# Kernel optimization log

Hardware: AMD Instinct MI355X
Metric: run time of the kernel (lower is better)

Reference implementation:

```python
import jax, jax.numpy as jnp
import numpy as np


def setup_inputs() -> dict:
    key = jax.random.key(0)
    k1, k2, k3, k4 = jax.random.split(key, 4)
    B, C_in, E = 8, 32, 100000
    C_out, K = 64, 5
    x = jax.random.normal(k1, (B, C_in, E, 1), dtype=jnp.float32)
    gemm_edges = jax.random.randint(k2, (B, E, 4), 0, E, dtype=jnp.int32)
    fan_in = C_in * K
    weight = jax.random.normal(k3, (C_out, C_in, 1, K), dtype=jnp.float32) / np.sqrt(fan_in)
    bias = jax.random.normal(k4, (C_out,), dtype=jnp.float32) * 0.01
    return {"x": x, "gemm_edges": gemm_edges, "weight": weight, "bias": bias}


def reference(x, gemm_edges, weight, bias):
    # x: (B, C, E, 1) edge features; gemm_edges: (B, E, 4) ring-neighbor indices
    xs = x[..., 0]                                   # (B, C, E)
    B, C, E = xs.shape
    # prepend self index -> (B, E, 5); +1 shifts into padded table (slot 0 = zero pad)
    idx_self = jnp.broadcast_to(jnp.arange(E, dtype=gemm_edges.dtype)[None, :, None], (B, E, 1))
    Gi = jnp.concatenate([idx_self, gemm_edges], axis=2) + 1  # (B, E, 5)
    xp = jnp.pad(xs, ((0, 0), (0, 0), (1, 0)))       # (B, C, E+1) with zero column at index 0
    # per-batch gather: f[b, c, e, k] = xp[b, c, Gi[b, e, k]]
    f = jnp.take_along_axis(xp, Gi.reshape(B, 1, E * 5), axis=2).reshape(B, C, E, 5)
    f0, f1, f2, f3, f4 = (f[..., i] for i in range(5))
    # symmetric functions for neighbor-order invariance
    G = jnp.stack([f0, f1 + f3, f2 + f4, jnp.abs(f1 - f3), jnp.abs(f2 - f4)], axis=3)  # (B, C, E, 5)
    # Conv2d kernel (1, 5) == contraction over (C, k), output (B, C_out, E, 1)
    out = jnp.einsum('bcek,ock->boe', G, weight[:, :, 0, :]) + bias[None, :, None]
    return out[..., None]
```

## Files before the change

### kernel.cpp

```cpp
#include <hip/hip_runtime.h>
#include <stdint.h>

#define E_TOTAL 100000
#define B_TOTAL 8
#define CIN 32
#define COUT 64
#define TILES 1563

typedef short bf16x8 __attribute__((ext_vector_type(8)));
typedef float f32x4  __attribute__((ext_vector_type(4)));
typedef int   i32x4  __attribute__((ext_vector_type(4)));
typedef unsigned u32x4 __attribute__((ext_vector_type(4)));

union U16x8 { u32x4 u; bf16x8 s; };

__device__ inline float blo(unsigned u) { return __uint_as_float(u << 16); }
__device__ inline float bhi(unsigned u) { return __uint_as_float(u & 0xffff0000u); }
__device__ inline unsigned bpack(float lo, float hi) {
    return (__float_as_uint(lo) >> 16) | (__float_as_uint(hi) & 0xffff0000u);
}
__device__ inline unsigned badd(unsigned a, unsigned b) {
    return bpack(blo(a) + blo(b), bhi(a) + bhi(b));
}
__device__ inline unsigned babsdiff(unsigned a, unsigned b) {
    return bpack(fabsf(blo(a) - blo(b)), fabsf(bhi(a) - bhi(b)));
}
__device__ inline u32x4 vadd4(u32x4 a, u32x4 b) {
    u32x4 r;
#pragma unroll
    for (int i = 0; i < 4; i++) r[i] = badd(a[i], b[i]);
    return r;
}
__device__ inline u32x4 vabsdiff4(u32x4 a, u32x4 b) {
    u32x4 r;
#pragma unroll
    for (int i = 0; i < 4; i++) r[i] = babsdiff(a[i], b[i]);
    return r;
}
__device__ inline unsigned rne16(float f) {
    unsigned b = __float_as_uint(f);
    b += 0x7fffu + ((b >> 16) & 1u);
    return b >> 16;
}

__global__ __launch_bounds__(256) void prep_transpose(
    const float* __restrict__ x, unsigned* __restrict__ xt,
    const float* __restrict__ w, unsigned short* __restrict__ wb) {
    const int tid = threadIdx.x;
    if (blockIdx.x >= TILES * 8) {
        for (int idx = tid; idx < 4 * 5 * 64 * 8; idx += 256) {
            int j = idx & 7;
            int lane = (idx >> 3) & 63;
            int tg = idx >> 9;
            int g = tg % 5;
            int t = tg / 5;
            int n = lane & 15, qq = lane >> 4;
            int o = n + 16 * t;
            int c = qq * 8 + j;
            wb[idx] = (unsigned short)rne16(w[(o * CIN + c) * 5 + g]);
        }
        return;
    }
    __shared__ float tbuf[CIN][65];
    const int b = blockIdx.x & 7;
    const int e0 = (blockIdx.x >> 3) * 64;
    const int el = tid & 63;
    const int cw = tid >> 6;
#pragma unroll
    for (int i = 0; i < 8; i++) {
        int c = cw * 8 + i;
        int e = e0 + el;
        float v = (e < E_TOTAL)
            ? __builtin_nontemporal_load(x + ((size_t)b * CIN + c) * E_TOTAL + e)
            : 0.f;
        tbuf[c][el] = v;
    }
    __syncthreads();
    const int c2 = tid & 15;
#pragma unroll
    for (int i = 0; i < 4; i++) {
        int el2 = (tid >> 4) * 4 + i;
        int e = e0 + el2;
        if (e < E_TOTAL) {
            unsigned lo = rne16(tbuf[c2 * 2][el2]);
            unsigned hi = rne16(tbuf[c2 * 2 + 1][el2]);
            xt[((size_t)b * E_TOTAL + e) * 16 + c2] = lo | (hi << 16);
        }
    }
}

__global__ __launch_bounds__(256) void meshconv_main(
    const unsigned short* __restrict__ xt,
    const int* __restrict__ ge,
    const u32x4* __restrict__ wb,
    const float* __restrict__ bias,
    float* __restrict__ out) {
    __shared__ u32x4 wlds[1280];
    const int tid = threadIdx.x;
    const int lane = tid & 63;
    const int wv = tid >> 6;
    const int b = blockIdx.x & 7;
    const int tile = blockIdx.x >> 3;
    const int e0 = tile * 64 + wv * 16;
    const int n = lane & 15;
    const int q = lane >> 4;
    const bool active = (e0 < E_TOTAL);
    const int em = active ? (e0 + n) : 0;

    i32x4 nid = __builtin_nontemporal_load(
        (const i32x4*)(ge + ((size_t)b * E_TOTAL + em) * 4));
    const unsigned short* xb = xt + (size_t)b * E_TOTAL * CIN;
    const int co = q * 8;
    u32x4 a0 = *(const u32x4*)(xb + (size_t)em * CIN + co);

#pragma unroll
    for (int k = 0; k < 5; k++) wlds[tid + k * 256] = wb[tid + k * 256];
    __syncthreads();

    u32x4 a1 = *(const u32x4*)(xb + (size_t)nid[0] * CIN + co);
    u32x4 a2 = *(const u32x4*)(xb + (size_t)nid[1] * CIN + co);
    u32x4 a3 = *(const u32x4*)(xb + (size_t)nid[2] * CIN + co);
    u32x4 a4 = *(const u32x4*)(xb + (size_t)nid[3] * CIN + co);

    u32x4 A[5];
    A[0] = a0;
    A[1] = vadd4(a1, a3);
    A[2] = vadd4(a2, a4);
    A[3] = vabsdiff4(a1, a3);
    A[4] = vabsdiff4(a2, a4);

    f32x4 acc[4];
#pragma unroll
    for (int t = 0; t < 4; t++)
#pragma unroll
        for (int r = 0; r < 4; r++) acc[t][r] = 0.f;

#pragma unroll
    for (int g = 0; g < 5; g++) {
        U16x8 av; av.u = A[g];
#pragma unroll
        for (int t = 0; t < 4; t++) {
            U16x8 bv; bv.u = wlds[(t * 5 + g) * 64 + lane];
            acc[t] = __builtin_amdgcn_mfma_f32_16x16x32_bf16(av.s, bv.s, acc[t], 0, 0, 0);
        }
    }

    if (active) {
#pragma unroll
        for (int t = 0; t < 4; t++) {
            const int o = n + 16 * t;
            f32x4 r = acc[t] + bias[o];
            __builtin_nontemporal_store(
                r, (f32x4*)(out + ((size_t)b * COUT + o) * E_TOTAL + e0 + q * 4));
        }
    }
}

__global__ __launch_bounds__(256) void meshconv_fallback(
    const float* __restrict__ x, const int* __restrict__ ge,
    const float* __restrict__ w, const float* __restrict__ bias,
    float* __restrict__ out) {
    __shared__ float f[5][32];
    __shared__ float G[5][32];
    __shared__ int idxs[4];
    const int e = blockIdx.x, b = blockIdx.y;
    const int tid = threadIdx.x;
    if (tid < 4) idxs[tid] = ge[((size_t)b * E_TOTAL + e) * 4 + tid];
    __syncthreads();
    if (tid < 160) {
        int k = tid >> 5, c = tid & 31;
        int src = (k == 0) ? e : idxs[k - 1];
        f[k][c] = x[((size_t)b * CIN + c) * E_TOTAL + src];
    }
    __syncthreads();
    if (tid < 32) {
        int c = tid;
        G[0][c] = f[0][c];
        G[1][c] = f[1][c] + f[3][c];
        G[2][c] = f[2][c] + f[4][c];
        G[3][c] = fabsf(f[1][c] - f[3][c]);
        G[4][c] = fabsf(f[2][c] - f[4][c]);
    }
    __syncthreads();
    if (tid < COUT) {
        float acc = bias[tid];
        for (int c = 0; c < CIN; c++)
#pragma unroll
            for (int g = 0; g < 5; g++)
                acc += G[g][c] * w[(tid * CIN + c) * 5 + g];
        out[((size_t)b * COUT + tid) * E_TOTAL + e] = acc;
    }
}

extern "C" void kernel_launch(void* const* d_in, const int* in_sizes, int n_in,
                              void* d_out, int out_size, void* d_ws, size_t ws_size,
                              hipStream_t stream) {
    const float* x = (const float*)d_in[0];
    const int* ge = (const int*)d_in[1];
    const float* w = (const float*)d_in[2];
    const float* bias = (const float*)d_in[3];
    float* out = (float*)d_out;

    const size_t xt_bytes = (size_t)B_TOTAL * E_TOTAL * CIN * 2;
    const size_t need = 65536 + xt_bytes;
    if (ws_size < need) {
        dim3 grid(E_TOTAL, B_TOTAL);
        meshconv_fallback<<<grid, 256, 0, stream>>>(x, ge, w, bias, out);
        return;
    }
    unsigned short* wb = (unsigned short*)d_ws;
    unsigned short* xt = (unsigned short*)((char*)d_ws + 65536);

    prep_transpose<<<TILES * 8 + 1, 256, 0, stream>>>(x, (unsigned*)xt, w, wb);
    meshconv_main<<<TILES * 8, 256, 0, stream>>>(xt, ge, (const u32x4*)wb, bias, out);
}
```

Before: 393.2 us.

## Make meshconv main kernel persistent with software-prefetched index and self loads

Replaces the one-tile-per-block launch with a persistent grid of 256 blocks per batch that loops over 128-edge units. Each wave now handles two 16-edge groups per iteration and prefetches the next unit's neighbor indices and self features while gathering the current ones. The weight LDS fill is paid once per block instead of once per tile. The cost is a much smaller grid and more live registers, which may reduce latency hiding for the random gathers.

```diff
diff --git a/kernel.cpp b/kernel.cpp
--- a/kernel.cpp
+++ b/kernel.cpp
@@ -6,6 +6,8 @@
 #define CIN 32
 #define COUT 64
 #define TILES 1563
+#define NUNITS 782
+#define NBLK 256
 
 typedef short bf16x8 __attribute__((ext_vector_type(8)));
 typedef float f32x4  __attribute__((ext_vector_type(4)));
@@ -54,8 +56,8 @@
             int tg = idx >> 9;
             int g = tg % 5;
             int t = tg / 5;
-            int n = lane & 15, qq = lane >> 4;
-            int o = n + 16 * t;
+            int nn = lane & 15, qq = lane >> 4;
+            int o = nn + 16 * t;
             int c = qq * 8 + j;
             wb[idx] = (unsigned short)rne16(w[(o * CIN + c) * 5 + g]);
         }
@@ -100,59 +102,102 @@
     const int lane = tid & 63;
     const int wv = tid >> 6;
     const int b = blockIdx.x & 7;
-    const int tile = blockIdx.x >> 3;
-    const int e0 = tile * 64 + wv * 16;
+    const int blk = blockIdx.x >> 3;
     const int n = lane & 15;
     const int q = lane >> 4;
-    const bool active = (e0 < E_TOTAL);
-    const int em = active ? (e0 + n) : 0;
-
-    i32x4 nid = __builtin_nontemporal_load(
-        (const i32x4*)(ge + ((size_t)b * E_TOTAL + em) * 4));
+    const int co = q * 8;
+
+#pragma unroll
+    for (int k = 0; k < 5; k++) wlds[tid + k * 256] = wb[tid + k * 256];
+    __syncthreads();
+
     const unsigned short* xb = xt + (size_t)b * E_TOTAL * CIN;
-    const int co = q * 8;
-    u32x4 a0 = *(const u32x4*)(xb + (size_t)em * CIN + co);
-
-#pragma unroll
-    for (int k = 0; k < 5; k++) wlds[tid + k * 256] = wb[tid + k * 256];
-    __syncthreads();
-
-    u32x4 a1 = *(const u32x4*)(xb + (size_t)nid[0] * CIN + co);
-    u32x4 a2 = *(const u32x4*)(xb + (size_t)nid[1] * CIN + co);
-    u32x4 a3 = *(const u32x4*)(xb + (size_t)nid[2] * CIN + co);
-    u32x4 a4 = *(const u32x4*)(xb + (size_t)nid[3] * CIN + co);
-
-    u32x4 A[5];
-    A[0] = a0;
-    A[1] = vadd4(a1, a3);
-    A[2] = vadd4(a2, a4);
-    A[3] = vabsdiff4(a1, a3);
-    A[4] = vabsdiff4(a2, a4);
-
-    f32x4 acc[4];
-#pragma unroll
-    for (int t = 0; t < 4; t++)
-#pragma unroll
-        for (int r = 0; r < 4; r++) acc[t][r] = 0.f;
-
-#pragma unroll
-    for (int g = 0; g < 5; g++) {
-        U16x8 av; av.u = A[g];
-#pragma unroll
-        for (int t = 0; t < 4; t++) {
-            U16x8 bv; bv.u = wlds[(t * 5 + g) * 64 + lane];
-            acc[t] = __builtin_amdgcn_mfma_f32_16x16x32_bf16(av.s, bv.s, acc[t], 0, 0, 0);
-        }
-    }
-
-    if (active) {
-#pragma unroll
-        for (int t = 0; t < 4; t++) {
-            const int o = n + 16 * t;
-            f32x4 r = acc[t] + bias[o];
-            __builtin_nontemporal_store(
-                r, (f32x4*)(out + ((size_t)b * COUT + o) * E_TOTAL + e0 + q * 4));
-        }
+    const int* geb = ge + (size_t)b * E_TOTAL * 4;
+    float bv[4];
+#pragma unroll
+    for (int t = 0; t < 4; t++) bv[t] = bias[n + 16 * t];
+
+    int u = blk;
+    int e0 = u * 128 + wv * 32;
+    bool act = (u < NUNITS) && (e0 < E_TOTAL);
+    i32x4 nid0, nid1;
+    u32x4 s0, s1;
+    if (act) {
+        nid0 = __builtin_nontemporal_load((const i32x4*)(geb + (size_t)(e0 + n) * 4));
+        nid1 = __builtin_nontemporal_load((const i32x4*)(geb + (size_t)(e0 + 16 + n) * 4));
+        s0 = *(const u32x4*)(xb + (size_t)(e0 + n) * CIN + co);
+        s1 = *(const u32x4*)(xb + (size_t)(e0 + 16 + n) * CIN + co);
+    }
+
+    for (; u < NUNITS; u += NBLK) {
+        const int un = u + NBLK;
+        const int e0n = un * 128 + wv * 32;
+        const bool actn = (un < NUNITS) && (e0n < E_TOTAL);
+
+        u32x4 g10, g20, g30, g40, g11, g21, g31, g41;
+        if (act) {
+            g10 = *(const u32x4*)(xb + (size_t)nid0[0] * CIN + co);
+            g20 = *(const u32x4*)(xb + (size_t)nid0[1] * CIN + co);
+            g30 = *(const u32x4*)(xb + (size_t)nid0[2] * CIN + co);
+            g40 = *(const u32x4*)(xb + (size_t)nid0[3] * CIN + co);
+            g11 = *(const u32x4*)(xb + (size_t)nid1[0] * CIN + co);
+            g21 = *(const u32x4*)(xb + (size_t)nid1[1] * CIN + co);
+            g31 = *(const u32x4*)(xb + (size_t)nid1[2] * CIN + co);
+            g41 = *(const u32x4*)(xb + (size_t)nid1[3] * CIN + co);
+        }
+        i32x4 nid0n, nid1n;
+        u32x4 s0n, s1n;
+        if (actn) {
+            nid0n = __builtin_nontemporal_load((const i32x4*)(geb + (size_t)(e0n + n) * 4));
+            nid1n = __builtin_nontemporal_load((const i32x4*)(geb + (size_t)(e0n + 16 + n) * 4));
+            s0n = *(const u32x4*)(xb + (size_t)(e0n + n) * CIN + co);
+            s1n = *(const u32x4*)(xb + (size_t)(e0n + 16 + n) * CIN + co);
+        }
+
+        if (act) {
+            u32x4 A0[5], A1[5];
+            A0[0] = s0;
+            A0[1] = vadd4(g10, g30);
+            A0[2] = vadd4(g20, g40);
+            A0[3] = vabsdiff4(g10, g30);
+            A0[4] = vabsdiff4(g20, g40);
+            A1[0] = s1;
+            A1[1] = vadd4(g11, g31);
+            A1[2] = vadd4(g21, g41);
+            A1[3] = vabsdiff4(g11, g31);
+            A1[4] = vabsdiff4(g21, g41);
+
+            f32x4 acc0[4], acc1[4];
+#pragma unroll
+            for (int t = 0; t < 4; t++)
+#pragma unroll
+                for (int r = 0; r < 4; r++) { acc0[t][r] = 0.f; acc1[t][r] = 0.f; }
+
+#pragma unroll
+            for (int g = 0; g < 5; g++) {
+                U16x8 av0; av0.u = A0[g];
+                U16x8 av1; av1.u = A1[g];
+#pragma unroll
+                for (int t = 0; t < 4; t++) {
+                    U16x8 bw; bw.u = wlds[(t * 5 + g) * 64 + lane];
+                    acc0[t] = __builtin_amdgcn_mfma_f32_16x16x32_bf16(av0.s, bw.s, acc0[t], 0, 0, 0);
+                    acc1[t] = __builtin_amdgcn_mfma_f32_16x16x32_bf16(av1.s, bw.s, acc1[t], 0, 0, 0);
+                }
+            }
+
+#pragma unroll
+            for (int t = 0; t < 4; t++) {
+                const int o = n + 16 * t;
+                float* orow = out + ((size_t)b * COUT + o) * E_TOTAL + e0 + q * 4;
+                f32x4 r0 = acc0[t] + bv[t];
+                f32x4 r1 = acc1[t] + bv[t];
+                __builtin_nontemporal_store(r0, (f32x4*)orow);
+                __builtin_nontemporal_store(r1, (f32x4*)(orow + 16));
+            }
+        }
+
+        nid0 = nid0n; nid1 = nid1n; s0 = s0n; s1 = s1n;
+        e0 = e0n; act = actn;
     }
 }
 
@@ -212,5 +257,5 @@
     unsigned short* xt = (unsigned short*)((char*)d_ws + 65536);
 
     prep_transpose<<<TILES * 8 + 1, 256, 0, stream>>>(x, (unsigned*)xt, w, wb);
-    meshconv_main<<<TILES * 8, 256, 0, stream>>>(xt, ge, (const u32x4*)wb, bias, out);
-}
+    meshconv_main<<<NBLK * 8, 256, 0, stream>>>(xt, ge, (const u32x4*)wb, bias, out);
+}
```

Measured after the change: 374.0 us. 4.9% less time.
